# Kernel optimization log

Hardware: AMD Instinct MI355X
Metric: run time of the kernel (lower is better)

Reference implementation:

```python
import jax, jax.numpy as jnp
import numpy as np

N_FEATURES = 26          # number of feature categories (FEATURE_AND_ENCODER entries)
VOCAB_PER_FEATURE = 50000  # ids in [f*V, (f+1)*V) belong to feature f
SLOTS_PER_FEATURE = 8
BATCH = 16384
EMBED = 32
VOCAB = N_FEATURES * VOCAB_PER_FEATURE


def setup_inputs() -> dict:
    key = jax.random.key(0)
    ks = jax.random.split(key, 8)
    P = N_FEATURES * SLOTS_PER_FEATURE  # 208 ids per row
    x = jax.random.randint(ks[0], (BATCH, P), 0, VOCAB, dtype=jnp.int64)
    table = jax.random.normal(ks[1], (VOCAB, EMBED), dtype=jnp.float32) * 0.1
    D = N_FEATURES * EMBED  # 832
    W0 = jax.random.normal(ks[2], (D, 64), dtype=jnp.float32) * (1.0 / np.sqrt(D))
    b0 = jax.random.normal(ks[3], (64,), dtype=jnp.float32) * 0.01
    W1 = jax.random.normal(ks[4], (64, 16), dtype=jnp.float32) * (1.0 / 8.0)
    b1 = jax.random.normal(ks[5], (16,), dtype=jnp.float32) * 0.01
    W2 = jax.random.normal(ks[6], (16, 1), dtype=jnp.float32) * 0.25
    return {"x": x, "table": table, "W0": W0, "b0": b0, "W1": W1, "b1": b1, "W2": W2}


def reference(x, table, W0, b0, W1, b1, W2):
    B = x.shape[0]
    # dynamic embedding lookup: [B, P, E]
    embeds = table[x]
    # category of each id (what encoder.match_category encodes): [B, P]
    cat = x // VOCAB_PER_FEATURE
    # mask+gather+reduce_sum per feature == one-hot segment sum over features
    onehot = jax.nn.one_hot(cat, N_FEATURES, dtype=table.dtype)  # [B, P, F]
    pooled = jnp.einsum('bpe,bpf->bfe', embeds, onehot)          # [B, F, E]
    feats = pooled.reshape(B, N_FEATURES * EMBED)                # concat of per-feature sums
    h = jax.nn.relu(feats @ W0 + b0)
    h = jax.nn.relu(h @ W1 + b1)
    logits = h @ W2
    return jax.nn.sigmoid(logits)
```

## Files before the change

kernel.cpp:

```cpp
#include <hip/hip_runtime.h>
#include <math.h>

#define BATCH 16384
#define PP    208
#define NF    26
#define VPF   50000u
#define EMB   32
#define DD    832
#define VOCAB (NF * 50000)

typedef __attribute__((ext_vector_type(8))) short short8v;
typedef __attribute__((ext_vector_type(4))) float float4v;

static __device__ __forceinline__ ushort f32_to_bf16(float f) {
    unsigned u = __builtin_bit_cast(unsigned, f);
    unsigned r = (u + 0x7fffu + ((u >> 16) & 1u)) >> 16;
    return (ushort)r;
}
static __device__ __forceinline__ unsigned pack_bf16x2(float lo, float hi) {
    return (unsigned)f32_to_bf16(lo) | ((unsigned)f32_to_bf16(hi) << 16);
}


__global__ __launch_bounds__(256) void prep_w0(const float* __restrict__ W0,
                                               ushort* __restrict__ w0p) {
    const int i = blockIdx.x * 256 + threadIdx.x;
    if (i < DD * 64) {
        const int j    = i & 7;
        const int lane = (i >> 3) & 63;
        const int w    = (i >> 9) & 3;
        const int kt   = i >> 11;
        const int k    = kt * 32 + (lane >> 4) * 8 + j;
        const int col  = w * 16 + (lane & 15);
        w0p[i] = f32_to_bf16(W0[(size_t)k * 64 + col]);
    }
}

__global__ __launch_bounds__(256, 4) void pool_f32(const int* __restrict__ x,
                                                   const float* __restrict__ table,
                                                   ushort* __restrict__ featsw) {
    __shared__ int   s_ids[PP];
    __shared__ float s_pool[DD];

    const int    tid = threadIdx.x;
    const size_t row = blockIdx.x;

    for (int i = tid; i < DD; i += 256) s_pool[i] = 0.0f;
    if (tid < PP / 4)
        reinterpret_cast<int4*>(s_ids)[tid] =
            reinterpret_cast<const int4*>(x + row * PP)[tid];
    __syncthreads();

    const int e  = tid & 31;
    const int p0 = (tid >> 5) * 26;
    float* pool  = s_pool + e;

#pragma unroll 1
    for (int b = 0; b < 26; b += 2) {
        const unsigned id0 = (unsigned)s_ids[p0 + b + 0];
        const unsigned id1 = (unsigned)s_ids[p0 + b + 1];
        const float v0 = table[(size_t)id0 * EMB + e];
        const float v1 = table[(size_t)id1 * EMB + e];
        atomicAdd(pool + (id0 / VPF) * EMB, v0);
        atomicAdd(pool + (id1 / VPF) * EMB, v1);
    }
    __syncthreads();

    if (tid < 104) {
        const int kt = tid >> 2;
        const int lk = tid & 3;
        const float* s = s_pool + kt * 32 + lk * 8;
        uint4 o;
        o.x = pack_bf16x2(s[0], s[1]);
        o.y = pack_bf16x2(s[2], s[3]);
        o.z = pack_bf16x2(s[4], s[5]);
        o.w = pack_bf16x2(s[6], s[7]);
        const size_t rb = row >> 4, lr = row & 15;
        ushort* dst = featsw + (((rb * 26 + kt) * 64) + lk * 16 + lr) * 8;
        *reinterpret_cast<uint4*>(dst) = o;
    }
}

__global__ __launch_bounds__(256) void mlp_kernel(const ushort* __restrict__ featsw,
                                                  const ushort* __restrict__ w0p,
                                                  const float* __restrict__ b0,
                                                  const float* __restrict__ W1,
                                                  const float* __restrict__ b1,
                                                  const float* __restrict__ W2,
                                                  float* __restrict__ out) {
    __shared__ float sH[16][65];
    __shared__ float sH1[16][17];

    const int tid  = threadIdx.x;
    const int w    = tid >> 6;
    const int lane = tid & 63;
    const int rb   = blockIdx.x;

    const ushort* A = featsw + ((size_t)rb * 26 * 64 + lane) * 8;
    const ushort* B = w0p + (size_t)(w * 64 + lane) * 8;

    float4v acc0 = (float4v){0.f, 0.f, 0.f, 0.f};
    float4v acc1 = (float4v){0.f, 0.f, 0.f, 0.f};

#pragma unroll
    for (int kt = 0; kt < 26; kt += 2) {
        const short8v a0 = *reinterpret_cast<const short8v*>(A + (size_t)kt * 512);
        const short8v b0v = *reinterpret_cast<const short8v*>(B + (size_t)kt * 2048);
        const short8v a1 = *reinterpret_cast<const short8v*>(A + (size_t)(kt + 1) * 512);
        const short8v b1v = *reinterpret_cast<const short8v*>(B + (size_t)(kt + 1) * 2048);
        acc0 = __builtin_amdgcn_mfma_f32_16x16x32_bf16(a0, b0v, acc0, 0, 0, 0);
        acc1 = __builtin_amdgcn_mfma_f32_16x16x32_bf16(a1, b1v, acc1, 0, 0, 0);
    }

    {
        const int   col = w * 16 + (lane & 15);
        const float bb  = b0[col];
#pragma unroll
        for (int r = 0; r < 4; ++r) {
            const int rr = (lane >> 4) * 4 + r;
            sH[rr][col] = fmaxf(acc0[r] + acc1[r] + bb, 0.f);
        }
    }
    __syncthreads();

    {
        const int r = tid >> 4, c = tid & 15;
        float a0 = b1[c];
#pragma unroll 8
        for (int k = 0; k < 64; ++k)
            a0 = fmaf(sH[r][k], W1[k * 16 + c], a0);
        sH1[r][c] = fmaxf(a0, 0.f);
    }
    __syncthreads();

    if (tid < 16) {
        float z = 0.f;
#pragma unroll
        for (int j = 0; j < 16; ++j) z = fmaf(sH1[tid][j], W2[j], z);
        out[(size_t)rb * 16 + tid] = 1.f / (1.f + expf(-z));
    }
}

extern "C" void kernel_launch(void* const* d_in, const int* in_sizes, int n_in,
                              void* d_out, int out_size, void* d_ws, size_t ws_size,
                              hipStream_t stream) {
    const int*   x     = (const int*)d_in[0];
    const float* table = (const float*)d_in[1];
    const float* W0    = (const float*)d_in[2];
    const float* b0    = (const float*)d_in[3];
    const float* W1    = (const float*)d_in[4];
    const float* b1    = (const float*)d_in[5];
    const float* W2    = (const float*)d_in[6];
    float*       out   = (float*)d_out;

    ushort* featsw = (ushort*)d_ws;
    ushort* w0p    = featsw + (size_t)BATCH * DD;

    prep_w0<<<(DD * 64 + 255) / 256, 256, 0, stream>>>(W0, w0p);
    pool_f32<<<BATCH, 256, 0, stream>>>(x, table, featsw);
    mlp_kernel<<<BATCH / 16, 256, 0, stream>>>(featsw, w0p, b0, W1, b1, W2, out);
}
```

Baseline: 744.2 us.

## Fuse pooling and MLP into one per-row kernel with fp32 scalar matmul

Result: slower. 762.0 us (+2.4%).

```diff
diff --git a/kernel.cpp b/kernel.cpp
--- a/kernel.cpp
+++ b/kernel.cpp
@@ -9,38 +9,19 @@
 #define DD    832
 #define VOCAB (NF * 50000)
 
-typedef __attribute__((ext_vector_type(8))) short short8v;
-typedef __attribute__((ext_vector_type(4))) float float4v;
-
-static __device__ __forceinline__ ushort f32_to_bf16(float f) {
-    unsigned u = __builtin_bit_cast(unsigned, f);
-    unsigned r = (u + 0x7fffu + ((u >> 16) & 1u)) >> 16;
-    return (ushort)r;
-}
-static __device__ __forceinline__ unsigned pack_bf16x2(float lo, float hi) {
-    return (unsigned)f32_to_bf16(lo) | ((unsigned)f32_to_bf16(hi) << 16);
-}
-
-
-__global__ __launch_bounds__(256) void prep_w0(const float* __restrict__ W0,
-                                               ushort* __restrict__ w0p) {
-    const int i = blockIdx.x * 256 + threadIdx.x;
-    if (i < DD * 64) {
-        const int j    = i & 7;
-        const int lane = (i >> 3) & 63;
-        const int w    = (i >> 9) & 3;
-        const int kt   = i >> 11;
-        const int k    = kt * 32 + (lane >> 4) * 8 + j;
-        const int col  = w * 16 + (lane & 15);
-        w0p[i] = f32_to_bf16(W0[(size_t)k * 64 + col]);
-    }
-}
-
-__global__ __launch_bounds__(256, 4) void pool_f32(const int* __restrict__ x,
-                                                   const float* __restrict__ table,
-                                                   ushort* __restrict__ featsw) {
+__global__ __launch_bounds__(256, 4) void fused_kernel(const int* __restrict__ x,
+                                                       const float* __restrict__ table,
+                                                       const float* __restrict__ W0,
+                                                       const float* __restrict__ b0,
+                                                       const float* __restrict__ W1,
+                                                       const float* __restrict__ b1,
+                                                       const float* __restrict__ W2,
+                                                       float* __restrict__ out) {
     __shared__ int   s_ids[PP];
     __shared__ float s_pool[DD];
+    __shared__ float s_part[4][64];
+    __shared__ float sH[64];
+    __shared__ float sH1[16];
 
     const int    tid = threadIdx.x;
     const size_t row = blockIdx.x;
@@ -51,93 +32,57 @@
             reinterpret_cast<const int4*>(x + row * PP)[tid];
     __syncthreads();
 
-    const int e  = tid & 31;
-    const int p0 = (tid >> 5) * 26;
-    float* pool  = s_pool + e;
+    {
+        const int e  = tid & 31;
+        const int p0 = (tid >> 5) * 26;
+        float* pool  = s_pool + e;
 
 #pragma unroll 1
-    for (int b = 0; b < 26; b += 2) {
-        const unsigned id0 = (unsigned)s_ids[p0 + b + 0];
-        const unsigned id1 = (unsigned)s_ids[p0 + b + 1];
-        const float v0 = table[(size_t)id0 * EMB + e];
-        const float v1 = table[(size_t)id1 * EMB + e];
-        atomicAdd(pool + (id0 / VPF) * EMB, v0);
-        atomicAdd(pool + (id1 / VPF) * EMB, v1);
-    }
-    __syncthreads();
-
-    if (tid < 104) {
-        const int kt = tid >> 2;
-        const int lk = tid & 3;
-        const float* s = s_pool + kt * 32 + lk * 8;
-        uint4 o;
-        o.x = pack_bf16x2(s[0], s[1]);
-        o.y = pack_bf16x2(s[2], s[3]);
-        o.z = pack_bf16x2(s[4], s[5]);
-        o.w = pack_bf16x2(s[6], s[7]);
-        const size_t rb = row >> 4, lr = row & 15;
-        ushort* dst = featsw + (((rb * 26 + kt) * 64) + lk * 16 + lr) * 8;
-        *reinterpret_cast<uint4*>(dst) = o;
-    }
-}
-
-__global__ __launch_bounds__(256) void mlp_kernel(const ushort* __restrict__ featsw,
-                                                  const ushort* __restrict__ w0p,
-                                                  const float* __restrict__ b0,
-                                                  const float* __restrict__ W1,
-                                                  const float* __restrict__ b1,
-                                                  const float* __restrict__ W2,
-                                                  float* __restrict__ out) {
-    __shared__ float sH[16][65];
-    __shared__ float sH1[16][17];
-
-    const int tid  = threadIdx.x;
-    const int w    = tid >> 6;
-    const int lane = tid & 63;
-    const int rb   = blockIdx.x;
-
-    const ushort* A = featsw + ((size_t)rb * 26 * 64 + lane) * 8;
-    const ushort* B = w0p + (size_t)(w * 64 + lane) * 8;
-
-    float4v acc0 = (float4v){0.f, 0.f, 0.f, 0.f};
-    float4v acc1 = (float4v){0.f, 0.f, 0.f, 0.f};
-
-#pragma unroll
-    for (int kt = 0; kt < 26; kt += 2) {
-        const short8v a0 = *reinterpret_cast<const short8v*>(A + (size_t)kt * 512);
-        const short8v b0v = *reinterpret_cast<const short8v*>(B + (size_t)kt * 2048);
-        const short8v a1 = *reinterpret_cast<const short8v*>(A + (size_t)(kt + 1) * 512);
-        const short8v b1v = *reinterpret_cast<const short8v*>(B + (size_t)(kt + 1) * 2048);
-        acc0 = __builtin_amdgcn_mfma_f32_16x16x32_bf16(a0, b0v, acc0, 0, 0, 0);
-        acc1 = __builtin_amdgcn_mfma_f32_16x16x32_bf16(a1, b1v, acc1, 0, 0, 0);
-    }
-
-    {
-        const int   col = w * 16 + (lane & 15);
-        const float bb  = b0[col];
-#pragma unroll
-        for (int r = 0; r < 4; ++r) {
-            const int rr = (lane >> 4) * 4 + r;
-            sH[rr][col] = fmaxf(acc0[r] + acc1[r] + bb, 0.f);
+        for (int b = 0; b < 26; b += 2) {
+            const unsigned id0 = (unsigned)s_ids[p0 + b + 0];
+            const unsigned id1 = (unsigned)s_ids[p0 + b + 1];
+            const float v0 = table[(size_t)id0 * EMB + e];
+            const float v1 = table[(size_t)id1 * EMB + e];
+            atomicAdd(pool + (id0 / VPF) * EMB, v0);
+            atomicAdd(pool + (id1 / VPF) * EMB, v1);
         }
     }
     __syncthreads();
 
     {
-        const int r = tid >> 4, c = tid & 15;
-        float a0 = b1[c];
+        const int c = tid & 63;
+        const int s = tid >> 6;
+        const int k0 = s * 208;
+        const float* w = W0 + (size_t)k0 * 64 + c;
+        float acc = 0.0f;
 #pragma unroll 8
-        for (int k = 0; k < 64; ++k)
-            a0 = fmaf(sH[r][k], W1[k * 16 + c], a0);
-        sH1[r][c] = fmaxf(a0, 0.f);
+        for (int kk = 0; kk < 208; ++kk)
+            acc = fmaf(s_pool[k0 + kk], w[(size_t)kk * 64], acc);
+        s_part[s][c] = acc;
+    }
+    __syncthreads();
+
+    if (tid < 64) {
+        const float h = s_part[0][tid] + s_part[1][tid] + s_part[2][tid] +
+                        s_part[3][tid] + b0[tid];
+        sH[tid] = fmaxf(h, 0.0f);
     }
     __syncthreads();
 
     if (tid < 16) {
-        float z = 0.f;
+        float a = b1[tid];
+#pragma unroll 8
+        for (int k = 0; k < 64; ++k)
+            a = fmaf(sH[k], W1[k * 16 + tid], a);
+        sH1[tid] = fmaxf(a, 0.0f);
+    }
+    __syncthreads();
+
+    if (tid == 0) {
+        float z = 0.0f;
 #pragma unroll
-        for (int j = 0; j < 16; ++j) z = fmaf(sH1[tid][j], W2[j], z);
-        out[(size_t)rb * 16 + tid] = 1.f / (1.f + expf(-z));
+        for (int j = 0; j < 16; ++j) z = fmaf(sH1[j], W2[j], z);
+        out[row] = 1.0f / (1.0f + expf(-z));
     }
 }
 
@@ -153,10 +98,5 @@
     const float* W2    = (const float*)d_in[6];
     float*       out   = (float*)d_out;
 
-    ushort* featsw = (ushort*)d_ws;
-    ushort* w0p    = featsw + (size_t)BATCH * DD;
-
-    prep_w0<<<(DD * 64 + 255) / 256, 256, 0, stream>>>(W0, w0p);
-    pool_f32<<<BATCH, 256, 0, stream>>>(x, table, featsw);
-    mlp_kernel<<<BATCH / 16, 256, 0, stream>>>(featsw, w0p, b0, W1, b1, W2, out);
+    fused_kernel<<<BATCH, 256, 0, stream>>>(x, table, W0, b0, W1, b1, W2, out);
 }
```
